# Kernel tuning notes

Measured on AMD Instinct MI355X. Metric: run time of the kernel, lower is better.

## Reference

```python
import jax, jax.numpy as jnp
import numpy as np

N = 200000  # number of mesh nodes (source hardcodes n; scaled to production)

def setup_inputs() -> dict:
    key = jax.random.key(0)
    ks = jax.random.split(key, 7)
    spatial = jax.random.normal(ks[0], (N, 64), dtype=jnp.float32)
    structural = jax.random.normal(ks[1], (N, 131), dtype=jnp.float32)
    neighbour = jax.random.randint(ks[2], (N, 3), 0, N, dtype=jnp.int64)
    # Conv1d(kernel_size=1) == linear layer; weights [out_c, in_c]
    Wc = jax.random.normal(ks[3], (256, 195), dtype=jnp.float32) * (1.0 / np.sqrt(195))
    bc = jax.random.normal(ks[4], (256,), dtype=jnp.float32) * 0.01
    Wa = jax.random.normal(ks[5], (256, 131), dtype=jnp.float32) * (1.0 / np.sqrt(131))
    ba = jax.random.normal(ks[6], (256,), dtype=jnp.float32) * 0.01
    return {"spatial": spatial, "structural": structural, "neighbour": neighbour,
            "Wc": Wc, "bc": bc, "Wa": Wa, "ba": ba}

def reference(spatial, structural, neighbour, Wc, bc, Wa, ba):
    # Combination1: concat(spatial[n,64], structural[n,131]) -> 1x1 conv (linear)
    a1 = jnp.concatenate([spatial, structural], axis=1)      # [n,195]
    out1 = jnp.einsum('nc,oc->no', a1, Wc) + bc               # [n,256]
    # Aggregation1: mean of self + 3 gathered neighbor feature vectors
    nbr_feats = structural[neighbour]                          # [n,3,131] gather
    vec4 = (structural + nbr_feats.sum(axis=1)) * 0.25        # [n,131]
    out2 = jnp.einsum('nc,oc->no', vec4, Wa) + ba             # [n,256]
    return (out1, out2)
```

## Files before the change

### kernel.cpp

```cpp
#include <hip/hip_runtime.h>
#include <hip/hip_bf16.h>

#define K1 195
#define K1P 224
#define K2 131
#define K2B 136
#define K2P 160
#define OC 256
#define BM 32
#define S1 232
#define S2 168
#define SO 260
#define THREADS 512

typedef __attribute__((ext_vector_type(4))) float f32x4;
typedef __attribute__((ext_vector_type(8))) short bf16x8;
typedef __attribute__((ext_vector_type(4))) short bf16x4;
typedef __attribute__((ext_vector_type(2))) short bf16x2;

__device__ __forceinline__ short f2b(float x) {
    __hip_bfloat16 h = __float2bfloat16(x);
    return *reinterpret_cast<short*>(&h);
}
__device__ __forceinline__ float b2f(short x) {
    return __uint_as_float(((unsigned)(unsigned short)x) << 16);
}

__global__ void prep_weights_v15(const float* __restrict__ Wc, const float* __restrict__ Wa,
                                 __hip_bfloat16* __restrict__ WcP, __hip_bfloat16* __restrict__ WaP) {
    int t = blockIdx.x * blockDim.x + threadIdx.x;
    const int total1 = OC * K1P;
    const int total2 = OC * K2P;
    if (t < total1) {
        int oc = t / K1P, k = t - oc * K1P;
        float v = (k < K1) ? Wc[oc * K1 + k] : 0.0f;
        WcP[t] = __float2bfloat16(v);
    } else if (t < total1 + total2) {
        int u = t - total1;
        int oc = u / K2P, k = u - oc * K2P;
        float v = (k < K2) ? Wa[oc * K2 + k] : 0.0f;
        WaP[u] = __float2bfloat16(v);
    }
}

__global__ void prep_structB_v15(const float* __restrict__ structural,
                                 __hip_bfloat16* __restrict__ structB, int n) {
    int idx = blockIdx.x * blockDim.x + threadIdx.x;
    const int ppr = K2B / 2;
    if (idx >= n * ppr) return;
    int r = idx / ppr;
    int c = (idx - r * ppr) * 2;
    float v0 = (c     < K2) ? structural[(size_t)r * K2 + c]     : 0.0f;
    float v1 = (c + 1 < K2) ? structural[(size_t)r * K2 + c + 1] : 0.0f;
    bf16x2 o;
    o[0] = f2b(v0);
    o[1] = f2b(v1);
    *(bf16x2*)((short*)structB + (size_t)r * K2B + c) = o;
}

template<bool USE_SB>
__global__ __launch_bounds__(THREADS) void fused_mesh_v15(
        const float* __restrict__ spatial,
        const float* __restrict__ structural,
        const __hip_bfloat16* __restrict__ structB,
        const int* __restrict__ neighbour,
        const __hip_bfloat16* __restrict__ WcP,
        const float* __restrict__ bc,
        const __hip_bfloat16* __restrict__ WaP,
        const float* __restrict__ ba,
        float* __restrict__ out1,
        float* __restrict__ out2,
        int n) {
    __shared__ union SMem {
        struct {
            short A1[BM][S1];
            short A2[BM][S2];
            int   nidx[BM * 3];
        } s;
        float ols[BM][SO];
    } smem;

    const int t = threadIdx.x;
    const int r0 = blockIdx.x * BM;

    if (t < BM * 3) {
        size_t gi = (size_t)r0 * 3 + t;
        smem.s.nidx[t] = (gi < (size_t)n * 3) ? neighbour[gi] : 0;
    }

    for (int e = t; e < BM * (K1P - K1); e += THREADS) {
        int r = e / (K1P - K1);
        int k = K1 + (e - r * (K1P - K1));
        smem.s.A1[r][k] = 0;
    }
    for (int e = t; e < BM * (K2P - K2); e += THREADS) {
        int r = e / (K2P - K2);
        int k = K2 + (e - r * (K2P - K2));
        smem.s.A2[r][k] = 0;
    }

    {
        int r  = t >> 4;
        int c0 = (t & 15) * 4;
        int rr = min(r0 + r, n - 1);
        f32x4 v = *(const f32x4*)(spatial + (size_t)rr * 64 + c0);
        bf16x4 o;
        #pragma unroll
        for (int j = 0; j < 4; ++j) o[j] = f2b(v[j]);
        *(bf16x4*)&smem.s.A1[r][c0] = o;
    }
    __syncthreads();

    if constexpr (USE_SB) {
        for (int u = t; u < BM * 17; u += THREADS) {
            int r = u / 17;
            int c = (u - r * 17) * 8;
            int rr = min(r0 + r, n - 1);
            const short* sb = (const short*)structB;
            bf16x8 vs = *(const bf16x8*)(sb + (size_t)rr * K2B + c);
            *(bf16x8*)&smem.s.A1[r][64 + c] = vs;
            int n0 = smem.s.nidx[r * 3 + 0];
            int n1 = smem.s.nidx[r * 3 + 1];
            int n2 = smem.s.nidx[r * 3 + 2];
            bf16x8 v0 = *(const bf16x8*)(sb + (size_t)n0 * K2B + c);
            bf16x8 v1 = *(const bf16x8*)(sb + (size_t)n1 * K2B + c);
            bf16x8 v2 = *(const bf16x8*)(sb + (size_t)n2 * K2B + c);
            bf16x8 o;
            #pragma unroll
            for (int j = 0; j < 8; ++j)
                o[j] = f2b((b2f(vs[j]) + b2f(v0[j]) + b2f(v1[j]) + b2f(v2[j])) * 0.25f);
            *(bf16x8*)&smem.s.A2[r][c] = o;
        }
    } else {
        for (int e = t; e < BM * K2; e += THREADS) {
            int r = e / K2;
            int k = e - r * K2;
            int rr = min(r0 + r, n - 1);
            float self = structural[(size_t)rr * K2 + k];
            int n0 = smem.s.nidx[r * 3 + 0];
            int n1 = smem.s.nidx[r * 3 + 1];
            int n2 = smem.s.nidx[r * 3 + 2];
            float v = self + structural[(size_t)n0 * K2 + k]
                           + structural[(size_t)n1 * K2 + k]
                           + structural[(size_t)n2 * K2 + k];
            smem.s.A1[r][64 + k] = f2b(self);
            smem.s.A2[r][k]      = f2b(v * 0.25f);
        }
    }
    __syncthreads();

    const int wid  = t >> 6;
    const int lane = t & 63;
    const int lr   = lane & 15;
    const int lkc  = lane >> 4;
    const int colBase = wid * 32;

    f32x4 acc1[2][2], acc2[2][2];
    #pragma unroll
    for (int i = 0; i < 2; ++i)
        #pragma unroll
        for (int j = 0; j < 2; ++j) {
            acc1[i][j] = (f32x4){0.f, 0.f, 0.f, 0.f};
            acc2[i][j] = (f32x4){0.f, 0.f, 0.f, 0.f};
        }

    #pragma unroll
    for (int ks = 0; ks < K1P; ks += 32) {
        bf16x8 a[2], b[2];
        #pragma unroll
        for (int rt = 0; rt < 2; ++rt)
            a[rt] = *(const bf16x8*)&smem.s.A1[rt * 16 + lr][ks + lkc * 8];
        #pragma unroll
        for (int ct = 0; ct < 2; ++ct) {
            int oc = colBase + ct * 16 + lr;
            b[ct] = *(const bf16x8*)(WcP + (size_t)oc * K1P + ks + lkc * 8);
        }
        #pragma unroll
        for (int rt = 0; rt < 2; ++rt)
            #pragma unroll
            for (int ct = 0; ct < 2; ++ct)
                acc1[ct][rt] = __builtin_amdgcn_mfma_f32_16x16x32_bf16(b[ct], a[rt], acc1[ct][rt], 0, 0, 0);
    }

    #pragma unroll
    for (int ks = 0; ks < K2P; ks += 32) {
        bf16x8 a[2], b[2];
        #pragma unroll
        for (int rt = 0; rt < 2; ++rt)
            a[rt] = *(const bf16x8*)&smem.s.A2[rt * 16 + lr][ks + lkc * 8];
        #pragma unroll
        for (int ct = 0; ct < 2; ++ct) {
            int oc = colBase + ct * 16 + lr;
            b[ct] = *(const bf16x8*)(WaP + (size_t)oc * K2P + ks + lkc * 8);
        }
        #pragma unroll
        for (int rt = 0; rt < 2; ++rt)
            #pragma unroll
            for (int ct = 0; ct < 2; ++ct)
                acc2[ct][rt] = __builtin_amdgcn_mfma_f32_16x16x32_bf16(b[ct], a[rt], acc2[ct][rt], 0, 0, 0);
    }

    __syncthreads();

    #pragma unroll
    for (int ct = 0; ct < 2; ++ct) {
        int oc0 = colBase + ct * 16 + lkc * 4;
        f32x4 b4 = *(const f32x4*)(bc + oc0);
        #pragma unroll
        for (int rt = 0; rt < 2; ++rt)
            *(f32x4*)&smem.ols[rt * 16 + lr][oc0] = acc1[ct][rt] + b4;
    }
    __syncthreads();
    #pragma unroll
    for (int i = 0; i < 4; ++i) {
        int row = wid * 4 + i;
        f32x4 v = *(const f32x4*)&smem.ols[row][lane * 4];
        int node = r0 + row;
        if (node < n)
            __builtin_nontemporal_store(v, (f32x4*)(out1 + (size_t)node * OC + lane * 4));
    }
    __syncthreads();

    #pragma unroll
    for (int ct = 0; ct < 2; ++ct) {
        int oc0 = colBase + ct * 16 + lkc * 4;
        f32x4 b4 = *(const f32x4*)(ba + oc0);
        #pragma unroll
        for (int rt = 0; rt < 2; ++rt)
            *(f32x4*)&smem.ols[rt * 16 + lr][oc0] = acc2[ct][rt] + b4;
    }
    __syncthreads();
    #pragma unroll
    for (int i = 0; i < 4; ++i) {
        int row = wid * 4 + i;
        f32x4 v = *(const f32x4*)&smem.ols[row][lane * 4];
        int node = r0 + row;
        if (node < n)
            __builtin_nontemporal_store(v, (f32x4*)(out2 + (size_t)node * OC + lane * 4));
    }
}

extern "C" void kernel_launch(void* const* d_in, const int* in_sizes, int n_in,
                              void* d_out, int out_size, void* d_ws, size_t ws_size,
                              hipStream_t stream) {
    const float* spatial    = (const float*)d_in[0];
    const float* structural = (const float*)d_in[1];
    const int*   neighbour  = (const int*)d_in[2];
    const float* Wc = (const float*)d_in[3];
    const float* bc = (const float*)d_in[4];
    const float* Wa = (const float*)d_in[5];
    const float* ba = (const float*)d_in[6];

    const int n = in_sizes[0] / 64;

    float* out1 = (float*)d_out;
    float* out2 = out1 + (size_t)n * OC;

    __hip_bfloat16* WcP = (__hip_bfloat16*)d_ws;
    __hip_bfloat16* WaP = WcP + OC * K1P;

    const size_t wbytes = (size_t)(OC * K1P + OC * K2P) * sizeof(__hip_bfloat16);
    const size_t sbytes = (size_t)n * K2B * sizeof(__hip_bfloat16);
    const bool use_sb = (ws_size >= wbytes + sbytes);
    __hip_bfloat16* structB = (__hip_bfloat16*)((char*)d_ws + wbytes);

    {
        const int total = OC * K1P + OC * K2P;
        prep_weights_v15<<<(total + 255) / 256, 256, 0, stream>>>(Wc, Wa, WcP, WaP);
    }
    const int grid = (n + BM - 1) / BM;
    if (use_sb) {
        const int totalp = n * (K2B / 2);
        prep_structB_v15<<<(totalp + 255) / 256, 256, 0, stream>>>(structural, structB, n);
        fused_mesh_v15<true><<<grid, THREADS, 0, stream>>>(spatial, structural, structB, neighbour,
                                                           WcP, bc, WaP, ba, out1, out2, n);
    } else {
        fused_mesh_v15<false><<<grid, THREADS, 0, stream>>>(spatial, structural, structB, neighbour,
                                                            WcP, bc, WaP, ba, out1, out2, n);
    }
}
```

Before: 183.2 us.

## Fuse structural bf16 conversion into out1 GEMM kernel, split out2 into second kernel

Result: faster. 166.9 us (-8.9%).

```diff
diff --git a/kernel.cpp b/kernel.cpp
--- a/kernel.cpp
+++ b/kernel.cpp
@@ -16,7 +16,6 @@
 typedef __attribute__((ext_vector_type(4))) float f32x4;
 typedef __attribute__((ext_vector_type(8))) short bf16x8;
 typedef __attribute__((ext_vector_type(4))) short bf16x4;
-typedef __attribute__((ext_vector_type(2))) short bf16x2;
 
 __device__ __forceinline__ short f2b(float x) {
     __hip_bfloat16 h = __float2bfloat16(x);
@@ -26,7 +25,7 @@
     return __uint_as_float(((unsigned)(unsigned short)x) << 16);
 }
 
-__global__ void prep_weights_v15(const float* __restrict__ Wc, const float* __restrict__ Wa,
+__global__ void prep_weights_v16(const float* __restrict__ Wc, const float* __restrict__ Wa,
                                  __hip_bfloat16* __restrict__ WcP, __hip_bfloat16* __restrict__ WaP) {
     int t = blockIdx.x * blockDim.x + threadIdx.x;
     const int total1 = OC * K1P;
@@ -43,26 +42,222 @@
     }
 }
 
-__global__ void prep_structB_v15(const float* __restrict__ structural,
-                                 __hip_bfloat16* __restrict__ structB, int n) {
-    int idx = blockIdx.x * blockDim.x + threadIdx.x;
-    const int ppr = K2B / 2;
-    if (idx >= n * ppr) return;
-    int r = idx / ppr;
-    int c = (idx - r * ppr) * 2;
-    float v0 = (c     < K2) ? structural[(size_t)r * K2 + c]     : 0.0f;
-    float v1 = (c + 1 < K2) ? structural[(size_t)r * K2 + c + 1] : 0.0f;
-    bf16x2 o;
-    o[0] = f2b(v0);
-    o[1] = f2b(v1);
-    *(bf16x2*)((short*)structB + (size_t)r * K2B + c) = o;
-}
-
-template<bool USE_SB>
-__global__ __launch_bounds__(THREADS) void fused_mesh_v15(
+__global__ __launch_bounds__(THREADS) void k1_out1_sb_v16(
         const float* __restrict__ spatial,
         const float* __restrict__ structural,
+        const __hip_bfloat16* __restrict__ WcP,
+        const float* __restrict__ bc,
+        float* __restrict__ out1,
+        __hip_bfloat16* __restrict__ structB,
+        int n) {
+    __shared__ union SMem {
+        short A1[BM][S1];
+        float ols[BM][SO];
+    } smem;
+
+    const int t = threadIdx.x;
+    const int r0 = blockIdx.x * BM;
+
+    for (int e = t; e < BM * (K1P - K1); e += THREADS) {
+        int r = e / (K1P - K1);
+        int k = K1 + (e - r * (K1P - K1));
+        smem.A1[r][k] = 0;
+    }
+
+    {
+        int r  = t >> 4;
+        int c0 = (t & 15) * 4;
+        int rr = min(r0 + r, n - 1);
+        f32x4 v = *(const f32x4*)(spatial + (size_t)rr * 64 + c0);
+        bf16x4 o;
+        #pragma unroll
+        for (int j = 0; j < 4; ++j) o[j] = f2b(v[j]);
+        *(bf16x4*)&smem.A1[r][c0] = o;
+    }
+
+    {
+        const float* sbase = structural + (size_t)r0 * K2;
+        const int nf4 = (BM * K2) / 4;
+        for (int f = t; f < nf4; f += THREADS) {
+            f32x4 v = *(const f32x4*)(sbase + (size_t)f * 4);
+            int g = f * 4;
+            #pragma unroll
+            for (int j = 0; j < 4; ++j) {
+                int gg = g + j;
+                int r = gg / K2;
+                int k = gg - r * K2;
+                smem.A1[r][64 + k] = f2b(v[j]);
+            }
+        }
+    }
+    __syncthreads();
+
+    for (int u = t; u < BM * 17; u += THREADS) {
+        int r = u / 17;
+        int c = (u - r * 17) * 8;
+        int node = r0 + r;
+        if (node < n) {
+            bf16x8 v = *(const bf16x8*)&smem.A1[r][64 + c];
+            *(bf16x8*)((short*)structB + (size_t)node * K2B + c) = v;
+        }
+    }
+
+    const int wid  = t >> 6;
+    const int lane = t & 63;
+    const int lr   = lane & 15;
+    const int lkc  = lane >> 4;
+    const int colBase = wid * 32;
+
+    f32x4 acc[2][2];
+    #pragma unroll
+    for (int i = 0; i < 2; ++i)
+        #pragma unroll
+        for (int j = 0; j < 2; ++j)
+            acc[i][j] = (f32x4){0.f, 0.f, 0.f, 0.f};
+
+    #pragma unroll
+    for (int ks = 0; ks < K1P; ks += 32) {
+        bf16x8 a[2], b[2];
+        #pragma unroll
+        for (int rt = 0; rt < 2; ++rt)
+            a[rt] = *(const bf16x8*)&smem.A1[rt * 16 + lr][ks + lkc * 8];
+        #pragma unroll
+        for (int ct = 0; ct < 2; ++ct) {
+            int oc = colBase + ct * 16 + lr;
+            b[ct] = *(const bf16x8*)(WcP + (size_t)oc * K1P + ks + lkc * 8);
+        }
+        #pragma unroll
+        for (int rt = 0; rt < 2; ++rt)
+            #pragma unroll
+            for (int ct = 0; ct < 2; ++ct)
+                acc[ct][rt] = __builtin_amdgcn_mfma_f32_16x16x32_bf16(b[ct], a[rt], acc[ct][rt], 0, 0, 0);
+    }
+
+    __syncthreads();
+
+    #pragma unroll
+    for (int ct = 0; ct < 2; ++ct) {
+        int oc0 = colBase + ct * 16 + lkc * 4;
+        f32x4 b4 = *(const f32x4*)(bc + oc0);
+        #pragma unroll
+        for (int rt = 0; rt < 2; ++rt)
+            *(f32x4*)&smem.ols[rt * 16 + lr][oc0] = acc[ct][rt] + b4;
+    }
+    __syncthreads();
+    #pragma unroll
+    for (int i = 0; i < 4; ++i) {
+        int row = wid * 4 + i;
+        f32x4 v = *(const f32x4*)&smem.ols[row][lane * 4];
+        int node = r0 + row;
+        if (node < n)
+            __builtin_nontemporal_store(v, (f32x4*)(out1 + (size_t)node * OC + lane * 4));
+    }
+}
+
+__global__ __launch_bounds__(THREADS) void k2_out2_v16(
         const __hip_bfloat16* __restrict__ structB,
+        const int* __restrict__ neighbour,
+        const __hip_bfloat16* __restrict__ WaP,
+        const float* __restrict__ ba,
+        float* __restrict__ out2,
+        int n) {
+    __shared__ union SMem {
+        struct {
+            short A2[BM][S2];
+            int   nidx[BM * 3];
+        } s;
+        float ols[BM][SO];
+    } smem;
+
+    const int t = threadIdx.x;
+    const int r0 = blockIdx.x * BM;
+
+    if (t < BM * 3) {
+        size_t gi = (size_t)r0 * 3 + t;
+        smem.s.nidx[t] = (gi < (size_t)n * 3) ? neighbour[gi] : 0;
+    } else if (t < BM * 3 + 96) {
+        int e = t - BM * 3;
+        int r = e / 3;
+        int c = K2B + (e - r * 3) * 8;
+        *(bf16x8*)&smem.s.A2[r][c] = (bf16x8){0, 0, 0, 0, 0, 0, 0, 0};
+    }
+    __syncthreads();
+
+    for (int u = t; u < BM * 17; u += THREADS) {
+        int r = u / 17;
+        int c = (u - r * 17) * 8;
+        int rr = min(r0 + r, n - 1);
+        const short* sb = (const short*)structB;
+        bf16x8 vs = *(const bf16x8*)(sb + (size_t)rr * K2B + c);
+        int n0 = smem.s.nidx[r * 3 + 0];
+        int n1 = smem.s.nidx[r * 3 + 1];
+        int n2 = smem.s.nidx[r * 3 + 2];
+        bf16x8 v0 = *(const bf16x8*)(sb + (size_t)n0 * K2B + c);
+        bf16x8 v1 = *(const bf16x8*)(sb + (size_t)n1 * K2B + c);
+        bf16x8 v2 = *(const bf16x8*)(sb + (size_t)n2 * K2B + c);
+        bf16x8 o;
+        #pragma unroll
+        for (int j = 0; j < 8; ++j)
+            o[j] = f2b((b2f(vs[j]) + b2f(v0[j]) + b2f(v1[j]) + b2f(v2[j])) * 0.25f);
+        *(bf16x8*)&smem.s.A2[r][c] = o;
+    }
+    __syncthreads();
+
+    const int wid  = t >> 6;
+    const int lane = t & 63;
+    const int lr   = lane & 15;
+    const int lkc  = lane >> 4;
+    const int colBase = wid * 32;
+
+    f32x4 acc[2][2];
+    #pragma unroll
+    for (int i = 0; i < 2; ++i)
+        #pragma unroll
+        for (int j = 0; j < 2; ++j)
+            acc[i][j] = (f32x4){0.f, 0.f, 0.f, 0.f};
+
+    #pragma unroll
+    for (int ks = 0; ks < K2P; ks += 32) {
+        bf16x8 a[2], b[2];
+        #pragma unroll
+        for (int rt = 0; rt < 2; ++rt)
+            a[rt] = *(const bf16x8*)&smem.s.A2[rt * 16 + lr][ks + lkc * 8];
+        #pragma unroll
+        for (int ct = 0; ct < 2; ++ct) {
+            int oc = colBase + ct * 16 + lr;
+            b[ct] = *(const bf16x8*)(WaP + (size_t)oc * K2P + ks + lkc * 8);
+        }
+        #pragma unroll
+        for (int rt = 0; rt < 2; ++rt)
+            #pragma unroll
+            for (int ct = 0; ct < 2; ++ct)
+                acc[ct][rt] = __builtin_amdgcn_mfma_f32_16x16x32_bf16(b[ct], a[rt], acc[ct][rt], 0, 0, 0);
+    }
+
+    __syncthreads();
+
+    #pragma unroll
+    for (int ct = 0; ct < 2; ++ct) {
+        int oc0 = colBase + ct * 16 + lkc * 4;
+        f32x4 b4 = *(const f32x4*)(ba + oc0);
+        #pragma unroll
+        for (int rt = 0; rt < 2; ++rt)
+            *(f32x4*)&smem.ols[rt * 16 + lr][oc0] = acc[ct][rt] + b4;
+    }
+    __syncthreads();
+    #pragma unroll
+    for (int i = 0; i < 4; ++i) {
+        int row = wid * 4 + i;
+        f32x4 v = *(const f32x4*)&smem.ols[row][lane * 4];
+        int node = r0 + row;
+        if (node < n)
+            __builtin_nontemporal_store(v, (f32x4*)(out2 + (size_t)node * OC + lane * 4));
+    }
+}
+
+__global__ __launch_bounds__(THREADS) void fused_mesh_v16fb(
+        const float* __restrict__ spatial,
+        const float* __restrict__ structural,
         const int* __restrict__ neighbour,
         const __hip_bfloat16* __restrict__ WcP,
         const float* __restrict__ bc,
@@ -87,7 +282,6 @@
         size_t gi = (size_t)r0 * 3 + t;
         smem.s.nidx[t] = (gi < (size_t)n * 3) ? neighbour[gi] : 0;
     }
-
     for (int e = t; e < BM * (K1P - K1); e += THREADS) {
         int r = e / (K1P - K1);
         int k = K1 + (e - r * (K1P - K1));
@@ -98,7 +292,6 @@
         int k = K2 + (e - r * (K2P - K2));
         smem.s.A2[r][k] = 0;
     }
-
     {
         int r  = t >> 4;
         int c0 = (t & 15) * 4;
@@ -110,42 +303,19 @@
         *(bf16x4*)&smem.s.A1[r][c0] = o;
     }
     __syncthreads();
-
-    if constexpr (USE_SB) {
-        for (int u = t; u < BM * 17; u += THREADS) {
-            int r = u / 17;
-            int c = (u - r * 17) * 8;
-            int rr = min(r0 + r, n - 1);
-            const short* sb = (const short*)structB;
-            bf16x8 vs = *(const bf16x8*)(sb + (size_t)rr * K2B + c);
-            *(bf16x8*)&smem.s.A1[r][64 + c] = vs;
-            int n0 = smem.s.nidx[r * 3 + 0];
-            int n1 = smem.s.nidx[r * 3 + 1];
-            int n2 = smem.s.nidx[r * 3 + 2];
-            bf16x8 v0 = *(const bf16x8*)(sb + (size_t)n0 * K2B + c);
-            bf16x8 v1 = *(const bf16x8*)(sb + (size_t)n1 * K2B + c);
-            bf16x8 v2 = *(const bf16x8*)(sb + (size_t)n2 * K2B + c);
-            bf16x8 o;
-            #pragma unroll
-            for (int j = 0; j < 8; ++j)
-                o[j] = f2b((b2f(vs[j]) + b2f(v0[j]) + b2f(v1[j]) + b2f(v2[j])) * 0.25f);
-            *(bf16x8*)&smem.s.A2[r][c] = o;
-        }
-    } else {
-        for (int e = t; e < BM * K2; e += THREADS) {
-            int r = e / K2;
-            int k = e - r * K2;
-            int rr = min(r0 + r, n - 1);
-            float self = structural[(size_t)rr * K2 + k];
-            int n0 = smem.s.nidx[r * 3 + 0];
-            int n1 = smem.s.nidx[r * 3 + 1];
-            int n2 = smem.s.nidx[r * 3 + 2];
-            float v = self + structural[(size_t)n0 * K2 + k]
-                           + structural[(size_t)n1 * K2 + k]
-                           + structural[(size_t)n2 * K2 + k];
-            smem.s.A1[r][64 + k] = f2b(self);
-            smem.s.A2[r][k]      = f2b(v * 0.25f);
-        }
+    for (int e = t; e < BM * K2; e += THREADS) {
+        int r = e / K2;
+        int k = e - r * K2;
+        int rr = min(r0 + r, n - 1);
+        float self = structural[(size_t)rr * K2 + k];
+        int n0 = smem.s.nidx[r * 3 + 0];
+        int n1 = smem.s.nidx[r * 3 + 1];
+        int n2 = smem.s.nidx[r * 3 + 2];
+        float v = self + structural[(size_t)n0 * K2 + k]
+                       + structural[(size_t)n1 * K2 + k]
+                       + structural[(size_t)n2 * K2 + k];
+        smem.s.A1[r][64 + k] = f2b(self);
+        smem.s.A2[r][k]      = f2b(v * 0.25f);
     }
     __syncthreads();
 
@@ -163,7 +333,6 @@
             acc1[i][j] = (f32x4){0.f, 0.f, 0.f, 0.f};
             acc2[i][j] = (f32x4){0.f, 0.f, 0.f, 0.f};
         }
-
     #pragma unroll
     for (int ks = 0; ks < K1P; ks += 32) {
         bf16x8 a[2], b[2];
@@ -181,7 +350,6 @@
             for (int ct = 0; ct < 2; ++ct)
                 acc1[ct][rt] = __builtin_amdgcn_mfma_f32_16x16x32_bf16(b[ct], a[rt], acc1[ct][rt], 0, 0, 0);
     }
-
     #pragma unroll
     for (int ks = 0; ks < K2P; ks += 32) {
         bf16x8 a[2], b[2];
@@ -199,9 +367,7 @@
             for (int ct = 0; ct < 2; ++ct)
                 acc2[ct][rt] = __builtin_amdgcn_mfma_f32_16x16x32_bf16(b[ct], a[rt], acc2[ct][rt], 0, 0, 0);
     }
-
-    __syncthreads();
-
+    __syncthreads();
     #pragma unroll
     for (int ct = 0; ct < 2; ++ct) {
         int oc0 = colBase + ct * 16 + lkc * 4;
@@ -220,7 +386,6 @@
             __builtin_nontemporal_store(v, (f32x4*)(out1 + (size_t)node * OC + lane * 4));
     }
     __syncthreads();
-
     #pragma unroll
     for (int ct = 0; ct < 2; ++ct) {
         int oc0 = colBase + ct * 16 + lkc * 4;
@@ -266,16 +431,15 @@
 
     {
         const int total = OC * K1P + OC * K2P;
-        prep_weights_v15<<<(total + 255) / 256, 256, 0, stream>>>(Wc, Wa, WcP, WaP);
+        prep_weights_v16<<<(total + 255) / 256, 256, 0, stream>>>(Wc, Wa, WcP, WaP);
     }
     const int grid = (n + BM - 1) / BM;
     if (use_sb) {
-        const int totalp = n * (K2B / 2);
-        prep_structB_v15<<<(totalp + 255) / 256, 256, 0, stream>>>(structural, structB, n);
-        fused_mesh_v15<true><<<grid, THREADS, 0, stream>>>(spatial, structural, structB, neighbour,
-                                                           WcP, bc, WaP, ba, out1, out2, n);
+        k1_out1_sb_v16<<<grid, THREADS, 0, stream>>>(spatial, structural, WcP, bc,
+                                                     out1, structB, n);
+        k2_out2_v16<<<grid, THREADS, 0, stream>>>(structB, neighbour, WaP, ba, out2, n);
     } else {
-        fused_mesh_v15<false><<<grid, THREADS, 0, stream>>>(spatial, structural, structB, neighbour,
-                                                            WcP, bc, WaP, ba, out1, out2, n);
-    }
-}
+        fused_mesh_v16fb<<<grid, THREADS, 0, stream>>>(spatial, structural, neighbour,
+                                                       WcP, bc, WaP, ba, out1, out2, n);
+    }
+}
```
